# Kernel tuning notes

Hardware: AMD Instinct MI355X
Metric: run time of the kernel (lower is better)

The kernel has to match this reference:

```python
import jax, jax.numpy as jnp
import numpy as np

B, T, S, D, H, HD, DFF, NB = 2, 2048, 2048, 768, 12, 64, 3072, 32
HID = H * HD
EPS = 1e-6
NEG = -1e9


def rmsnorm(x, w):
    # T5 RMSNorm: no mean subtraction, no bias
    var = jnp.mean(jnp.square(x), axis=-1, keepdims=True)
    return x * jax.lax.rsqrt(var + EPS) * w


def sdpa(h, kv, m, wq, wk, wv, wo):
    # h: [B,Tq,D], kv: [B,Tk,D], m: additive mask broadcastable to [B,H,Tq,Tk]
    b, tq, _ = h.shape
    tk = kv.shape[1]
    q = (h @ wq).reshape(b, tq, H, HD)
    k = (kv @ wk).reshape(b, tk, H, HD)
    v = (kv @ wv).reshape(b, tk, H, HD)
    scores = jnp.einsum('bthd,bshd->bhts', q, k) + m  # scale=1.0 (T5)
    p = jax.nn.softmax(scores, axis=-1)
    y = jnp.einsum('bhts,bshd->bthd', p, v).reshape(b, tq, HID)
    return y @ wo


def setup_inputs() -> dict:
    key = jax.random.key(0)
    ks = jax.random.split(key, 16)
    x = jax.random.normal(ks[0], (B, T, D), dtype=jnp.float32)
    # causal additive mask for decoder self-attention
    causal = jnp.tril(jnp.ones((T, T), dtype=bool))
    mask = jnp.broadcast_to(jnp.where(causal, 0.0, NEG)[None, None], (B, 1, T, T)).astype(jnp.float32)
    relative_position = jax.random.randint(ks[1], (1, 1, T, T), 0, NB)
    encoder_hidden_states = jax.random.normal(ks[2], (B, S, D), dtype=jnp.float32)
    encoder_attention_mask = jnp.zeros((B, 1, T, S), dtype=jnp.float32)
    sc = 0.02
    p = {
        'sn_w': jnp.ones((D,), jnp.float32),
        'wq': sc * jax.random.normal(ks[3], (D, HID)),
        'wk': sc * jax.random.normal(ks[4], (D, HID)),
        'wv': sc * jax.random.normal(ks[5], (D, HID)),
        'wo': sc * jax.random.normal(ks[6], (HID, D)),
        'rel_emb': sc * jax.random.normal(ks[7], (NB, H)),
        'cn_w': jnp.ones((D,), jnp.float32),
        'cwq': sc * jax.random.normal(ks[8], (D, HID)),
        'cwk': sc * jax.random.normal(ks[9], (D, HID)),
        'cwv': sc * jax.random.normal(ks[10], (D, HID)),
        'cwo': sc * jax.random.normal(ks[11], (HID, D)),
        'pn_w': jnp.ones((D,), jnp.float32),
        'ffn_wi': sc * jax.random.normal(ks[12], (D, DFF)),
        'ffn_wo': sc * jax.random.normal(ks[13], (DFF, D)),
    }
    return dict(x=x, mask=mask, relative_position=relative_position,
                encoder_hidden_states=encoder_hidden_states,
                encoder_attention_mask=encoder_attention_mask, **p)


def reference(x, mask, relative_position, encoder_hidden_states, encoder_attention_mask,
              sn_w, wq, wk, wv, wo, rel_emb, cn_w, cwq, cwk, cwv, cwo, pn_w, ffn_wi, ffn_wo):
    # self-attention with relative-position bias added into additive mask
    h = rmsnorm(x, sn_w)
    # rel_emb[relative_position]: [1,1,T,T,H] -> permute(0,1,4,2,3) -> squeeze(0) -> [1,H,T,T]
    position_bias = jnp.transpose(rel_emb[relative_position], (0, 1, 4, 2, 3))[0]
    self_mask = mask + position_bias
    y = sdpa(h, h, self_mask, wq, wk, wv, wo)
    attn_out = y + x
    # cross-attention (no relative bias -> zeros position bias)
    enc_dec_position_bias = jnp.zeros_like(encoder_attention_mask)
    h2 = rmsnorm(attn_out, cn_w)
    y2 = sdpa(h2, encoder_hidden_states, encoder_attention_mask + enc_dec_position_bias,
              cwq, cwk, cwv, cwo)
    attn_out = y2 + attn_out
    # T5 FFN: relu(x @ wi) @ wo, pre-norm, residual
    hn = rmsnorm(attn_out, pn_w)
    ff = jax.nn.relu(hn @ ffn_wi) @ ffn_wo
    return (attn_out + ff, position_bias, enc_dec_position_bias)
```

## Files before the change

kernel.cpp:

```cpp
#include <hip/hip_runtime.h>
#include <hip/hip_bf16.h>
#include <stdint.h>

#define T5_B   2
#define T5_T   2048
#define T5_S   2048
#define T5_D   768
#define T5_H   12
#define T5_HD  64
#define T5_DFF 3072
#define T5_NB  32
#define NROW   4096

typedef __attribute__((ext_vector_type(8))) short bf16x8;
typedef __attribute__((ext_vector_type(4))) short short4v;
typedef __attribute__((ext_vector_type(4))) float f32x4;

__device__ __forceinline__ unsigned short f2bf(float x) {
  unsigned int u = __float_as_uint(x);
  unsigned int r = (u + 0x7FFFu + ((u >> 16) & 1u)) >> 16;
  return (unsigned short)r;
}

__device__ __forceinline__ void load_lds16(const void* g, void* l) {
  __builtin_amdgcn_global_load_lds(
      (__attribute__((address_space(1))) void*)(const_cast<void*>(g)),
      (__attribute__((address_space(3))) void*)(l), 16, 0, 0);
}

__device__ __forceinline__ unsigned cvt_pk_bf16(float lo_, float hi_) {
  unsigned d;
  asm("v_cvt_pk_bf16_f32 %0, %1, %2" : "=v"(d) : "v"(lo_), "v"(hi_));
  return d;
}

__device__ __forceinline__ f32x4 mfma16(short4v a, short4v b, f32x4 c) {
#if __has_builtin(__builtin_amdgcn_mfma_f32_16x16x16bf16_1k)
  return __builtin_amdgcn_mfma_f32_16x16x16bf16_1k(a, b, c, 0, 0, 0);
#else
  asm volatile("v_mfma_f32_16x16x16_bf16 %0, %1, %2, %0" : "+v"(c) : "v"(a), "v"(b));
  return c;
#endif
}

__device__ __forceinline__ int xcd_swz(int f, int nwg) {
  int q8 = nwg >> 3, r8 = nwg & 7, xcd = f & 7, base = f >> 3;
  return (xcd < r8 ? xcd * (q8 + 1) : r8 * (q8 + 1) + (xcd - r8) * q8) + base;
}

template <int TM, int TN, int EPI, int NBUF>
__device__ __forceinline__ void gemm_body(
    int f, int gx, int nwg,
    const unsigned short* __restrict__ A, const unsigned short* __restrict__ Bt,
    void* __restrict__ C, const float* __restrict__ res, int N, int K,
    unsigned short* LDS, unsigned short* vtp = nullptr, int vcol0 = 0) {
  constexpr int WR = (TM >= 128) ? 2 : 1;
  constexpr int WC = 4 / WR;
  constexpr int AM = TM / WR / 16;
  constexpr int AN = TN / WC / 16;
  constexpr int CHA = TM / 8, CHB = TN / 8, CPW = (CHA + CHB) / 4;
  constexpr int BUFSH = (TM + TN) * 64;
  constexpr int DEPTH = NBUF - 1;
  const int tid = threadIdx.x, lane = tid & 63, wv = tid >> 6;
  const int lo = lane & 15, hi = lane >> 4;
  const int wr = wv / WC, wc = wv % WC;
  const int wg = xcd_swz(f, nwg);
  const int m0 = (wg / gx) * TM, n0 = (wg % gx) * TN;

  f32x4 acc[AM][AN];
#pragma unroll
  for (int i = 0; i < AM; ++i)
#pragma unroll
    for (int j = 0; j < AN; ++j) acc[i][j] = f32x4{0.f, 0.f, 0.f, 0.f};

  const int srr  = lane >> 3;
  const int scol = ((lane & 7) ^ srr) * 8;

  auto stage = [&](int k0, int bsel) {
    unsigned short* Ab = LDS + bsel * BUFSH;
    unsigned short* Bb = Ab + TM * 64;
#pragma unroll
    for (int j = 0; j < CPW; ++j) {
      int c = wv * CPW + j;
      if (c < CHA)
        load_lds16(A + (size_t)(m0 + c * 8 + srr) * K + k0 + scol, Ab + c * 512);
      else {
        int c2 = c - CHA;
        load_lds16(Bt + (size_t)(n0 + c2 * 8 + srr) * K + k0 + scol, Bb + c2 * 512);
      }
    }
  };

  const int nIt = K >> 6;
#pragma unroll
  for (int p = 0; p < DEPTH; ++p)
    if (p < nIt) stage(p << 6, p % NBUF);

  for (int it = 0; it < nIt; ++it) {
    const int bsel = it % NBUF;
    if (it + DEPTH < nIt) {
      stage((it + DEPTH) << 6, (it + DEPTH) % NBUF);
      asm volatile("s_waitcnt vmcnt(%0)" :: "n"(DEPTH * CPW) : "memory");
    } else if (it + 1 < nIt) {
      asm volatile("s_waitcnt vmcnt(%0)" :: "n"(CPW) : "memory");
    } else {
      asm volatile("s_waitcnt vmcnt(0)" ::: "memory");
    }
    __builtin_amdgcn_s_barrier();
    __builtin_amdgcn_sched_barrier(0);
    const unsigned short* Ab = LDS + bsel * BUFSH;
    const unsigned short* Bb = Ab + TM * 64;
#pragma unroll
    for (int kk = 0; kk < 2; ++kk) {
      bf16x8 af[AM], bfr[AN];
#pragma unroll
      for (int i = 0; i < AM; ++i) {
        int row = wr * (AM * 16) + i * 16 + lo;
        unsigned by = (unsigned)(row * 128) + ((unsigned)(((kk * 4 + hi) ^ (row & 7))) << 4);
        af[i] = *(const bf16x8*)((const char*)Ab + by);
      }
#pragma unroll
      for (int j = 0; j < AN; ++j) {
        int row = wc * (AN * 16) + j * 16 + lo;
        unsigned by = (unsigned)(row * 128) + ((unsigned)(((kk * 4 + hi) ^ (row & 7))) << 4);
        bfr[j] = *(const bf16x8*)((const char*)Bb + by);
      }
      __builtin_amdgcn_s_setprio(1);
#pragma unroll
      for (int i = 0; i < AM; ++i)
#pragma unroll
        for (int j = 0; j < AN; ++j)
          acc[i][j] = __builtin_amdgcn_mfma_f32_16x16x32_bf16(af[i], bfr[j], acc[i][j], 0, 0, 0);
      __builtin_amdgcn_s_setprio(0);
    }
    __builtin_amdgcn_sched_barrier(0);
    __builtin_amdgcn_s_barrier();
  }

#pragma unroll
  for (int mi = 0; mi < AM; ++mi)
#pragma unroll
    for (int ni = 0; ni < AN; ++ni) {
      int row = m0 + wr * (AM * 16) + mi * 16 + hi * 4;
      int col = n0 + wc * (AN * 16) + ni * 16 + lo;
      if (EPI == 3 && col >= vcol0) {
        int cc = col - vcol0, hh = cc >> 6, dd = cc & 63;
        int bb = row >> 11, tt = row & 2047;
        unsigned long long pk = (unsigned long long)f2bf(acc[mi][ni][0])
                              | ((unsigned long long)f2bf(acc[mi][ni][1]) << 16)
                              | ((unsigned long long)f2bf(acc[mi][ni][2]) << 32)
                              | ((unsigned long long)f2bf(acc[mi][ni][3]) << 48);
        *(unsigned long long*)(vtp + ((size_t)((bb * 12 + hh) * 64 + dd)) * 2048 + tt) = pk;
      } else {
#pragma unroll
        for (int r = 0; r < 4; ++r) {
          float v = acc[mi][ni][r];
          size_t idx = (size_t)(row + r) * N + col;
          if (EPI == 0 || EPI == 3) {
            ((unsigned short*)C)[idx] = f2bf(v);
          } else if (EPI == 1) {
            ((float*)C)[idx] = v + res[idx];
          } else {
            ((unsigned short*)C)[idx] = f2bf(fmaxf(v, 0.0f));
          }
        }
      }
    }
}

template <int TM, int TN, int EPI, int NBUF>
__global__ __launch_bounds__(256)
void gemm_bt(const unsigned short* __restrict__ A, const unsigned short* __restrict__ Bt,
             void* __restrict__ C, const float* __restrict__ res, int N, int K) {
  __shared__ __align__(16) unsigned short LDS[NBUF * (TM + TN) * 64];
  int f = blockIdx.y * gridDim.x + blockIdx.x;
  gemm_body<TM, TN, EPI, NBUF>(f, gridDim.x, gridDim.x * gridDim.y, A, Bt, C, res, N, K, LDS);
}

struct PrepArgs {
  const float* wsrc[10];
  unsigned short* wdst[10];
  const float* enc; unsigned short* encb;
  const int* rp; unsigned char* rp8;
  const float* x; const float* snw; unsigned short* normb;
};

__global__ __launch_bounds__(256)
void prep_kernel(PrepArgs a) {
  __shared__ __align__(16) float tile[32][33];
  const int bid = blockIdx.x, tid = threadIdx.x;
  if (bid < 9216) {
    int widx, rem, Kd, Nd;
    if (bid < 4608)      { widx = bid / 576; rem = bid % 576;  Kd = 768;  Nd = 768;  }
    else if (bid < 6912) { widx = 8;         rem = bid - 4608; Kd = 768;  Nd = 3072; }
    else                 { widx = 9;         rem = bid - 6912; Kd = 3072; Nd = 768;  }
    const float* W = a.wsrc[widx];
    unsigned short* Wt = a.wdst[widx];
    int nb = Nd / 32;
    int n0 = (rem % nb) * 32, k0 = (rem / nb) * 32;
    int tx = tid & 31, ty = tid >> 5;
#pragma unroll
    for (int i = 0; i < 32; i += 8)
      tile[ty + i][tx] = W[(size_t)(k0 + ty + i) * Nd + n0 + tx];
    __syncthreads();
#pragma unroll
    for (int i = 0; i < 32; i += 8)
      Wt[(size_t)(n0 + ty + i) * Kd + k0 + tx] = f2bf(tile[tx][ty + i]);
  } else if (bid < 12288) {
    int i = (bid - 9216) * 256 + tid;
    float4 v = ((const float4*)a.enc)[i];
    unsigned long long pk = (unsigned long long)f2bf(v.x)
                          | ((unsigned long long)f2bf(v.y) << 16)
                          | ((unsigned long long)f2bf(v.z) << 32)
                          | ((unsigned long long)f2bf(v.w) << 48);
    *(unsigned long long*)(a.encb + (size_t)i * 4) = pk;
  } else if (bid < 13312) {
    int idx = (bid - 12288) * 256 + tid;
    const int4* src = (const int4*)(a.rp + (size_t)idx * 16);
    int4 v0 = src[0], v1 = src[1], v2 = src[2], v3 = src[3];
    uint4 o;
    o.x = (v0.x & 31) | ((v0.y & 31) << 8) | ((v0.z & 31) << 16) | ((v0.w & 31) << 24);
    o.y = (v1.x & 31) | ((v1.y & 31) << 8) | ((v1.z & 31) << 16) | ((v1.w & 31) << 24);
    o.z = (v2.x & 31) | ((v2.y & 31) << 8) | ((v2.z & 31) << 16) | ((v2.w & 31) << 24);
    o.w = (v3.x & 31) | ((v3.y & 31) << 8) | ((v3.z & 31) << 16) | ((v3.w & 31) << 24);
    ((uint4*)a.rp8)[idx] = o;
  } else {
    int row = bid - 13312;
    const float* r = a.x + (size_t)row * 768;
    float x0 = r[tid], x1 = r[tid + 256], x2 = r[tid + 512];
    float s = x0 * x0 + x1 * x1 + x2 * x2;
#pragma unroll
    for (int off = 32; off > 0; off >>= 1) s += __shfl_xor(s, off);
    float* wsm = &tile[0][0];
    int lane = tid & 63, wvv = tid >> 6;
    if (lane == 0) wsm[wvv] = s;
    __syncthreads();
    float tot = wsm[0] + wsm[1] + wsm[2] + wsm[3];
    float rinv = rsqrtf(tot * (1.0f / 768.0f) + 1e-6f);
    unsigned short* o = a.normb + (size_t)row * 768;
    o[tid]       = f2bf(x0 * rinv * a.snw[tid]);
    o[tid + 256] = f2bf(x1 * rinv * a.snw[tid + 256]);
    o[tid + 512] = f2bf(x2 * rinv * a.snw[tid + 512]);
  }
}

__global__ __launch_bounds__(256)
void rmsnorm_kernel(const float* __restrict__ in, const float* __restrict__ w,
                    unsigned short* __restrict__ out) {
  int row = blockIdx.x, tid = threadIdx.x;
  const float* r = in + (size_t)row * 768;
  float x0 = r[tid], x1 = r[tid + 256], x2 = r[tid + 512];
  float s = x0 * x0 + x1 * x1 + x2 * x2;
#pragma unroll
  for (int off = 32; off > 0; off >>= 1) s += __shfl_xor(s, off);
  __shared__ float ws_[4];
  int lane = tid & 63, wv = tid >> 6;
  if (lane == 0) ws_[wv] = s;
  __syncthreads();
  float tot = ws_[0] + ws_[1] + ws_[2] + ws_[3];
  float rinv = rsqrtf(tot * (1.0f / 768.0f) + 1e-6f);
  unsigned short* o = out + (size_t)row * 768;
  o[tid]       = f2bf(x0 * rinv * w[tid]);
  o[tid + 256] = f2bf(x1 * rinv * w[tid + 256]);
  o[tid + 512] = f2bf(x2 * rinv * w[tid + 512]);
}

struct Stage1Args {
  const unsigned short *normb, *wqkvT, *encb, *wckvT;
  unsigned short *qkv, *ckv, *vT1, *vT2;
  const int* rp; const float* rel;
  float *out1, *out2;
};

__global__ __launch_bounds__(256)
void stage1_kernel(Stage1Args a) {
  __shared__ __align__(16) unsigned short LDS[32768];
  const int bid = blockIdx.x, tid = threadIdx.x;
  if (bid < 576) {
    gemm_body<128, 128, 3, 2>(bid, 18, 576, a.normb, a.wqkvT, a.qkv, nullptr, 2304, 768,
                              LDS, a.vT1, 1536);
  } else if (bid < 960) {
    gemm_body<128, 128, 3, 2>(bid - 576, 12, 384, a.encb, a.wckvT, a.ckv, nullptr, 1536, 768,
                              LDS, a.vT2, 768);
  } else {
    const int p = bid - 960;
    float* rl = (float*)LDS;
    for (int i = tid; i < 384; i += 256) rl[i] = a.rel[i];
    __syncthreads();
    int t = p >> 1;
    int s = (p & 1) * 1024 + tid * 4;
    int4 nb = *(const int4*)(a.rp + (size_t)t * 2048 + s);
#pragma unroll
    for (int h = 0; h < 12; ++h) {
      float4 v = make_float4(rl[nb.x * 12 + h], rl[nb.y * 12 + h],
                             rl[nb.z * 12 + h], rl[nb.w * 12 + h]);
      *(float4*)(a.out1 + ((size_t)h * 2048 + t) * 2048 + s) = v;
    }
    size_t zbase = ((size_t)p * 256 + tid) * 8;
    float4 z = make_float4(0.f, 0.f, 0.f, 0.f);
    *(float4*)(a.out2 + zbase)     = z;
    *(float4*)(a.out2 + zbase + 4) = z;
  }
}

template <bool SELF>
__device__ __forceinline__ void attn_qcomp(
    const bf16x8& qf0, const bf16x8& qf1, f32x4* Oc, float& m_, float& l_,
    const unsigned* nb4, const float* rel_l, int qrow, bool edge, int s0,
    const unsigned short* Kb, const unsigned short* Vb, int lo, int hi) {
  f32x4 S[4];
  __builtin_amdgcn_s_setprio(1);
#pragma unroll
  for (int ct = 0; ct < 4; ++ct) {
    int krow = ct * 16 + lo;
    unsigned by0 = ((unsigned)(krow * 128 + hi * 16))      ^ ((unsigned)(krow & 7) << 4);
    unsigned by1 = ((unsigned)(krow * 128 + 64 + hi * 16)) ^ ((unsigned)(krow & 7) << 4);
    bf16x8 kf0 = *(const bf16x8*)((const char*)Kb + by0);
    bf16x8 kf1 = *(const bf16x8*)((const char*)Kb + by1);
    f32x4 sa = f32x4{0.f, 0.f, 0.f, 0.f};
    sa = __builtin_amdgcn_mfma_f32_16x16x32_bf16(kf0, qf0, sa, 0, 0, 0);
    sa = __builtin_amdgcn_mfma_f32_16x16x32_bf16(kf1, qf1, sa, 0, 0, 0);
    S[ct] = sa;
  }
  __builtin_amdgcn_s_setprio(0);

  if constexpr (SELF) {
#pragma unroll
    for (int ct = 0; ct < 4; ++ct) {
#pragma unroll
      for (int r = 0; r < 4; ++r) {
        int s = s0 + ct * 16 + hi * 4 + r;
        float sc = S[ct][r] + rel_l[(nb4[ct] >> (8 * r)) & 31u];
        if (edge && s > qrow) sc = -1e30f;
        S[ct][r] = sc;
      }
    }
  }

  float tm = S[0][0];
#pragma unroll
  for (int ct = 0; ct < 4; ++ct)
#pragma unroll
    for (int r = 0; r < 4; ++r) tm = fmaxf(tm, S[ct][r]);
  tm = fmaxf(tm, __shfl_xor(tm, 16));
  tm = fmaxf(tm, __shfl_xor(tm, 32));
  float mn = fmaxf(m_, tm);
  float alpha = __expf(m_ - mn);
  float rs = 0.f;
#pragma unroll
  for (int ct = 0; ct < 4; ++ct)
#pragma unroll
    for (int r = 0; r < 4; ++r) { float e = __expf(S[ct][r] - mn); S[ct][r] = e; rs += e; }
  rs += __shfl_xor(rs, 16);
  rs += __shfl_xor(rs, 32);
  l_ = l_ * alpha + rs;
  if (tm > m_) {
#pragma unroll
    for (int dt = 0; dt < 4; ++dt)
#pragma unroll
      for (int r = 0; r < 4; ++r) Oc[dt][r] *= alpha;
  }
  m_ = mn;

  short4v pf[4];
#pragma unroll
  for (int ct = 0; ct < 4; ++ct) {
    union { unsigned u[2]; short4v s; } cv;
    cv.u[0] = cvt_pk_bf16(S[ct][0], S[ct][1]);
    cv.u[1] = cvt_pk_bf16(S[ct][2], S[ct][3]);
    pf[ct] = cv.s;
  }

  __builtin_amdgcn_s_setprio(1);
#pragma unroll
  for (int dt = 0; dt < 4; ++dt) {
    int vrow = dt * 16 + lo;
#pragma unroll
    for (int ct = 0; ct < 4; ++ct) {
      unsigned vb = ((unsigned)(vrow * 128 + ct * 32 + hi * 8)) ^ ((unsigned)(vrow & 7) << 4);
      short4v vf = *(const short4v*)((const char*)Vb + vb);
      Oc[dt] = mfma16(vf, pf[ct], Oc[dt]);
    }
  }
  __builtin_amdgcn_s_setprio(0);
}

__device__ __forceinline__ void attn_store(f32x4* Oc, float l_, unsigned short* yr) {
  float inv = 1.0f / l_;
#pragma unroll
  for (int dt = 0; dt < 4; ++dt) {
    unsigned long long pk = (unsigned long long)f2bf(Oc[dt][0] * inv)
                          | ((unsigned long long)f2bf(Oc[dt][1] * inv) << 16)
                          | ((unsigned long long)f2bf(Oc[dt][2] * inv) << 32)
                          | ((unsigned long long)f2bf(Oc[dt][3] * inv) << 48);
    *(unsigned long long*)(yr + dt * 16) = pk;
  }
}

__global__ __launch_bounds__(256)
void attn_self_kernel(const unsigned short* __restrict__ qp,
                      const unsigned short* __restrict__ kp,
                      const unsigned short* __restrict__ vT,
                      const unsigned char* __restrict__ rp8,
                      const float* __restrict__ rel_emb,
                      unsigned short* __restrict__ yp) {
  __shared__ __align__(16) unsigned short Kls[2][4096];
  __shared__ __align__(16) unsigned short Vls[2][4096];
  __shared__ float rel_l[32];

  const int tid = threadIdx.x, lane = tid & 63, wv = tid >> 6;
  const int lo = lane & 15, hi = lane >> 4;
  const int wg = xcd_swz(blockIdx.x + 16 * (blockIdx.y + 12 * blockIdx.z), 384);
  const int xq = wg & 15, h = (wg >> 4) % 12, b = (wg >> 4) / 12;
  const int qta = xq, qtb = 31 - xq;
  const int ntiles = qtb + 1;

  if (tid < 32) rel_l[tid] = rel_emb[tid * 12 + h];

  const int qA = qta * 64 + wv * 16 + lo;
  const int qB = qtb * 64 + wv * 16 + lo;
  const unsigned short* qrA = qp + (size_t)(b * T5_T + qA) * 2304 + h * 64 + hi * 8;
  const unsigned short* qrB = qp + (size_t)(b * T5_T + qB) * 2304 + h * 64 + hi * 8;
  const bf16x8 qa0 = *(const bf16x8*)qrA;
  const bf16x8 qa1 = *(const bf16x8*)(qrA + 32);
  const bf16x8 qb0 = *(const bf16x8*)qrB;
  const bf16x8 qb1 = *(const bf16x8*)(qrB + 32);
  const unsigned char* rpqA = rp8 + (size_t)qA * 2048 + hi * 4;
  const unsigned char* rpqB = rp8 + (size_t)qB * 2048 + hi * 4;

  f32x4 OA[4], OB[4];
  float mA = -3.0e38f, lA = 0.f, mB = -3.0e38f, lB = 0.f;
#pragma unroll
  for (int i = 0; i < 4; ++i) { OA[i] = f32x4{0.f, 0.f, 0.f, 0.f}; OB[i] = f32x4{0.f, 0.f, 0.f, 0.f}; }

  const int krr = lane >> 3;
  const int kd0 = ((lane & 7) ^ krr) * 8;

  auto stage = [&](int kt, int bsel) {
    const int s0 = kt * 64;
#pragma unroll
    for (int j = 0; j < 2; ++j) {
      int c = wv * 2 + j;
      int rr = c * 8 + krr;
      load_lds16(kp + (size_t)(b * 2048 + s0 + rr) * 2304 + h * 64 + kd0, &Kls[bsel][c * 512]);
      load_lds16(vT + (size_t)((b * 12 + h) * 64 + rr) * 2048 + s0 + kd0,  &Vls[bsel][c * 512]);
    }
  };

  stage(0, 0);

  for (int kt = 0; kt < ntiles; ++kt) {
    const int bsel = kt & 1;
    const int s0 = kt * 64;
    asm volatile("s_waitcnt vmcnt(0)" ::: "memory");
    __syncthreads();
    unsigned nbA[4], nbB[4];
    if (kt <= qta) {
#pragma unroll
      for (int ct = 0; ct < 4; ++ct) nbA[ct] = *(const unsigned*)(rpqA + s0 + ct * 16);
    }
#pragma unroll
    for (int ct = 0; ct < 4; ++ct) nbB[ct] = *(const unsigned*)(rpqB + s0 + ct * 16);
    if (kt + 1 < ntiles) stage(kt + 1, bsel ^ 1);

    const unsigned short* Kb = &Kls[bsel][0];
    const unsigned short* Vb = &Vls[bsel][0];

    if (kt <= qta)
      attn_qcomp<true>(qa0, qa1, OA, mA, lA, nbA, rel_l, qA, kt == qta, s0, Kb, Vb, lo, hi);
    attn_qcomp<true>(qb0, qb1, OB, mB, lB, nbB, rel_l, qB, kt == qtb, s0, Kb, Vb, lo, hi);
  }

#if !__has_builtin(__builtin_amdgcn_mfma_f32_16x16x16bf16_1k)
  asm volatile("s_nop 7\n\ts_nop 7" ::: );
#endif

  attn_store(OA, lA, yp + (size_t)(b * T5_T + qA) * 768 + h * 64 + hi * 4);
  attn_store(OB, lB, yp + (size_t)(b * T5_T + qB) * 768 + h * 64 + hi * 4);
}

__global__ __launch_bounds__(256)
void attn_cross_kernel(const unsigned short* __restrict__ qp,
                       const unsigned short* __restrict__ kp,
                       const unsigned short* __restrict__ vT,
                       unsigned short* __restrict__ yp) {
  __shared__ __align__(16) unsigned short Kls[2][4096];
  __shared__ __align__(16) unsigned short Vls[2][4096];

  const int tid = threadIdx.x, lane = tid & 63, wv = tid >> 6;
  const int lo = lane & 15, hi = lane >> 4;
  const int wg = xcd_swz(blockIdx.x + 32 * (blockIdx.y + 12 * blockIdx.z), 768);
  const int xq = wg & 31, h = (wg >> 5) % 12, b = (wg >> 5) / 12;

  const int q = xq * 64 + wv * 16 + lo;
  const unsigned short* qr = qp + (size_t)(b * T5_T + q) * 768 + h * 64 + hi * 8;
  const bf16x8 qf0 = *(const bf16x8*)qr;
  const bf16x8 qf1 = *(const bf16x8*)(qr + 32);

  f32x4 Oc[4];
  float m_ = -3.0e38f, l_ = 0.f;
#pragma unroll
  for (int i = 0; i < 4; ++i) Oc[i] = f32x4{0.f, 0.f, 0.f, 0.f};

  const int krr = lane >> 3;
  const int kd0 = ((lane & 7) ^ krr) * 8;

  auto stage = [&](int kt, int bsel) {
    const int s0 = kt * 64;
#pragma unroll
    for (int j = 0; j < 2; ++j) {
      int c = wv * 2 + j;
      int rr = c * 8 + krr;
      load_lds16(kp + (size_t)(b * 2048 + s0 + rr) * 1536 + h * 64 + kd0, &Kls[bsel][c * 512]);
      load_lds16(vT + (size_t)((b * 12 + h) * 64 + rr) * 2048 + s0 + kd0, &Vls[bsel][c * 512]);
    }
  };

  stage(0, 0);

  for (int kt = 0; kt < 32; ++kt) {
    const int bsel = kt & 1;
    asm volatile("s_waitcnt vmcnt(0)" ::: "memory");
    __syncthreads();
    if (kt + 1 < 32) stage(kt + 1, bsel ^ 1);
    attn_qcomp<false>(qf0, qf1, Oc, m_, l_, nullptr, nullptr, 0, false, kt * 64,
                      &Kls[bsel][0], &Vls[bsel][0], lo, hi);
  }

#if !__has_builtin(__builtin_amdgcn_mfma_f32_16x16x16bf16_1k)
  asm volatile("s_nop 7\n\ts_nop 7" ::: );
#endif

  attn_store(Oc, l_, yp + (size_t)(b * T5_T + q) * 768 + h * 64 + hi * 4);
}

extern "C" void kernel_launch(void* const* d_in, const int* in_sizes, int n_in,
                              void* d_out, int out_size, void* d_ws, size_t ws_size,
                              hipStream_t stream) {
  (void)in_sizes; (void)n_in; (void)out_size; (void)ws_size;
  const float* x    = (const float*)d_in[0];
  const int*   rp   = (const int*)d_in[2];
  const float* enc  = (const float*)d_in[3];
  const float* sn_w = (const float*)d_in[5];
  const float* wq   = (const float*)d_in[6];
  const float* wk   = (const float*)d_in[7];
  const float* wvw  = (const float*)d_in[8];
  const float* wo   = (const float*)d_in[9];
  const float* rel  = (const float*)d_in[10];
  const float* cn_w = (const float*)d_in[11];
  const float* cwq  = (const float*)d_in[12];
  const float* cwk  = (const float*)d_in[13];
  const float* cwv  = (const float*)d_in[14];
  const float* cwo  = (const float*)d_in[15];
  const float* pn_w = (const float*)d_in[16];
  const float* wi   = (const float*)d_in[17];
  const float* wo2  = (const float*)d_in[18];

  float* out0 = (float*)d_out;
  float* out1 = out0 + (size_t)NROW * T5_D;
  float* out2 = out1 + (size_t)T5_H * T5_T * T5_T;

  char* ws = (char*)d_ws;
  size_t off = 0;
  auto alloc = [&](size_t bytes) { char* p = ws + off; off += (bytes + 255) & ~(size_t)255; return p; };
  unsigned short* wqkvT = (unsigned short*)alloc((size_t)2304 * 768 * 2);
  unsigned short* woT   = (unsigned short*)alloc((size_t)768 * 768 * 2);
  unsigned short* wckvT = (unsigned short*)alloc((size_t)1536 * 768 * 2);
  unsigned short* wcqT  = (unsigned short*)alloc((size_t)768 * 768 * 2);
  unsigned short* wcoT  = (unsigned short*)alloc((size_t)768 * 768 * 2);
  unsigned short* wiT   = (unsigned short*)alloc((size_t)3072 * 768 * 2);
  unsigned short* woT2  = (unsigned short*)alloc((size_t)768 * 3072 * 2);
  unsigned short* normb = (unsigned short*)alloc((size_t)NROW * 768 * 2);
  unsigned short* encb  = (unsigned short*)alloc((size_t)NROW * 768 * 2);
  unsigned short* ybuf  = (unsigned short*)alloc((size_t)NROW * 768 * 2);
  unsigned short* cq    = (unsigned short*)alloc((size_t)NROW * 768 * 2);
  float*          attn  = (float*)alloc((size_t)NROW * 768 * 4);
  unsigned char*  rp8p  = (unsigned char*)alloc((size_t)2048 * 2048);
  unsigned short* qkv   = (unsigned short*)alloc((size_t)NROW * 2304 * 2);
  unsigned short* ckv   = (unsigned short*)alloc((size_t)NROW * 1536 * 2);
  unsigned short* vT1   = (unsigned short*)alloc((size_t)24 * 64 * 2048 * 2);
  unsigned short* vT2   = (unsigned short*)alloc((size_t)24 * 64 * 2048 * 2);
  unsigned short* ffh   = (unsigned short*)alloc((size_t)NROW * 3072 * 2);

  dim3 blk(256);

  {
    PrepArgs pa;
    pa.wsrc[0] = wq;  pa.wdst[0] = wqkvT;
    pa.wsrc[1] = wk;  pa.wdst[1] = wqkvT + 768 * 768;
    pa.wsrc[2] = wvw; pa.wdst[2] = wqkvT + 2 * 768 * 768;
    pa.wsrc[3] = wo;  pa.wdst[3] = woT;
    pa.wsrc[4] = cwk; pa.wdst[4] = wckvT;
    pa.wsrc[5] = cwv; pa.wdst[5] = wckvT + 768 * 768;
    pa.wsrc[6] = cwq; pa.wdst[6] = wcqT;
    pa.wsrc[7] = cwo; pa.wdst[7] = wcoT;
    pa.wsrc[8] = wi;  pa.wdst[8] = wiT;
    pa.wsrc[9] = wo2; pa.wdst[9] = woT2;
    pa.enc = enc; pa.encb = encb; pa.rp = rp; pa.rp8 = rp8p;
    pa.x = x; pa.snw = sn_w; pa.normb = normb;
    prep_kernel<<<17408, blk, 0, stream>>>(pa);
  }

  {
    Stage1Args sa;
    sa.normb = normb; sa.wqkvT = wqkvT; sa.encb = encb; sa.wckvT = wckvT;
    sa.qkv = qkv; sa.ckv = ckv; sa.vT1 = vT1; sa.vT2 = vT2;
    sa.rp = rp; sa.rel = rel; sa.out1 = out1; sa.out2 = out2;
    stage1_kernel<<<5056, blk, 0, stream>>>(sa);
  }

  attn_self_kernel<<<dim3(16, 12, 2), blk, 0, stream>>>(qkv, qkv + 768, vT1, rp8p, rel, ybuf);
  gemm_bt<64, 64, 1, 3><<<dim3(12, 64), blk, 0, stream>>>(ybuf, woT, attn, x, 768, 768);

  rmsnorm_kernel<<<NROW, blk, 0, stream>>>(attn, cn_w, normb);
  gemm_bt<64, 64, 0, 3><<<dim3(12, 64), blk, 0, stream>>>(normb, wcqT, cq, nullptr, 768, 768);
  attn_cross_kernel<<<dim3(32, 12, 2), blk, 0, stream>>>(cq, ckv, vT2, ybuf);
  gemm_bt<64, 64, 1, 3><<<dim3(12, 64), blk, 0, stream>>>(ybuf, wcoT, attn, attn, 768, 768);

  rmsnorm_kernel<<<NROW, blk, 0, stream>>>(attn, pn_w, normb);
  gemm_bt<128, 128, 2, 2><<<dim3(24, 32), blk, 0, stream>>>(normb, wiT, ffh, nullptr, 3072, 768);
  gemm_bt<64, 64, 1, 3><<<dim3(12, 64), blk, 0, stream>>>(ffh, woT2, out0, attn, 768, 3072);
}
```

Baseline: 352.2 us.

## Use 32x32 MFMA for large GEMM tiles and fold log2e into Q for exp2 softmax

GEMMs with 128x128 tiles now use the 32x32x16 bf16 MFMA with a 2x2 accumulator layout per wave, instead of 16x16x32 fragments. This is meant to cut LDS fragment reads and instruction count per unit of work. Separately, Q projections (self and cross) and the relative-position bias table are pre-scaled by log2(e) in their epilogues, so the attention softmax can call raw v_exp_f32 instead of __expf. This removes a multiply per exponential, at the cost of bf16 rounding on the pre-scaled Q.

```diff
diff --git a/kernel.cpp b/kernel.cpp
--- a/kernel.cpp
+++ b/kernel.cpp
@@ -12,14 +12,23 @@
 #define T5_NB  32
 #define NROW   4096
 
+#define LOG2E 1.4426950408889634f
+
 typedef __attribute__((ext_vector_type(8))) short bf16x8;
 typedef __attribute__((ext_vector_type(4))) short short4v;
 typedef __attribute__((ext_vector_type(4))) float f32x4;
+typedef __attribute__((ext_vector_type(16))) float f32x16;
 
 __device__ __forceinline__ unsigned short f2bf(float x) {
   unsigned int u = __float_as_uint(x);
   unsigned int r = (u + 0x7FFFu + ((u >> 16) & 1u)) >> 16;
   return (unsigned short)r;
+}
+
+__device__ __forceinline__ float fexp2(float x) {
+  float d;
+  asm("v_exp_f32 %0, %1" : "=v"(d) : "v"(x));
+  return d;
 }
 
 __device__ __forceinline__ void load_lds16(const void* g, void* l) {
@@ -53,7 +62,8 @@
     int f, int gx, int nwg,
     const unsigned short* __restrict__ A, const unsigned short* __restrict__ Bt,
     void* __restrict__ C, const float* __restrict__ res, int N, int K,
-    unsigned short* LDS, unsigned short* vtp = nullptr, int vcol0 = 0) {
+    unsigned short* LDS, unsigned short* vtp = nullptr, int vcol0 = 0, int qe = 0) {
+  constexpr bool USE32 = (TM >= 128 && TN >= 128);
   constexpr int WR = (TM >= 128) ? 2 : 1;
   constexpr int WC = 4 / WR;
   constexpr int AM = TM / WR / 16;
@@ -63,15 +73,26 @@
   constexpr int DEPTH = NBUF - 1;
   const int tid = threadIdx.x, lane = tid & 63, wv = tid >> 6;
   const int lo = lane & 15, hi = lane >> 4;
+  const int l5 = lane >> 5, l31 = lane & 31;
   const int wr = wv / WC, wc = wv % WC;
   const int wg = xcd_swz(f, nwg);
   const int m0 = (wg / gx) * TM, n0 = (wg % gx) * TN;
 
-  f32x4 acc[AM][AN];
-#pragma unroll
-  for (int i = 0; i < AM; ++i)
-#pragma unroll
-    for (int j = 0; j < AN; ++j) acc[i][j] = f32x4{0.f, 0.f, 0.f, 0.f};
+  f32x4 acc[USE32 ? 1 : AM][USE32 ? 1 : AN];
+  f32x16 acc32[USE32 ? 2 : 1][USE32 ? 2 : 1];
+  if (USE32) {
+#pragma unroll
+    for (int i = 0; i < (USE32 ? 2 : 1); ++i)
+#pragma unroll
+      for (int j = 0; j < (USE32 ? 2 : 1); ++j)
+#pragma unroll
+        for (int r = 0; r < 16; ++r) acc32[i][j][r] = 0.f;
+  } else {
+#pragma unroll
+    for (int i = 0; i < (USE32 ? 1 : AM); ++i)
+#pragma unroll
+      for (int j = 0; j < (USE32 ? 1 : AN); ++j) acc[i][j] = f32x4{0.f, 0.f, 0.f, 0.f};
+  }
 
   const int srr  = lane >> 3;
   const int scol = ((lane & 7) ^ srr) * 8;
@@ -110,48 +131,104 @@
     __builtin_amdgcn_sched_barrier(0);
     const unsigned short* Ab = LDS + bsel * BUFSH;
     const unsigned short* Bb = Ab + TM * 64;
-#pragma unroll
-    for (int kk = 0; kk < 2; ++kk) {
-      bf16x8 af[AM], bfr[AN];
-#pragma unroll
-      for (int i = 0; i < AM; ++i) {
-        int row = wr * (AM * 16) + i * 16 + lo;
-        unsigned by = (unsigned)(row * 128) + ((unsigned)(((kk * 4 + hi) ^ (row & 7))) << 4);
-        af[i] = *(const bf16x8*)((const char*)Ab + by);
+    if (USE32) {
+#pragma unroll
+      for (int kk = 0; kk < 4; ++kk) {
+        bf16x8 af[2], bfr[2];
+#pragma unroll
+        for (int i = 0; i < 2; ++i) {
+          int row = wr * 64 + i * 32 + l31;
+          unsigned by = (unsigned)(row * 128) + ((unsigned)(((kk * 2 + l5) ^ (row & 7))) << 4);
+          af[i] = *(const bf16x8*)((const char*)Ab + by);
+        }
+#pragma unroll
+        for (int j = 0; j < 2; ++j) {
+          int row = wc * 64 + j * 32 + l31;
+          unsigned by = (unsigned)(row * 128) + ((unsigned)(((kk * 2 + l5) ^ (row & 7))) << 4);
+          bfr[j] = *(const bf16x8*)((const char*)Bb + by);
+        }
+        __builtin_amdgcn_s_setprio(1);
+#pragma unroll
+        for (int i = 0; i < 2; ++i)
+#pragma unroll
+          for (int j = 0; j < 2; ++j)
+            acc32[i][j] = __builtin_amdgcn_mfma_f32_32x32x16_bf16(af[i], bfr[j], acc32[i][j], 0, 0, 0);
+        __builtin_amdgcn_s_setprio(0);
       }
-#pragma unroll
-      for (int j = 0; j < AN; ++j) {
-        int row = wc * (AN * 16) + j * 16 + lo;
-        unsigned by = (unsigned)(row * 128) + ((unsigned)(((kk * 4 + hi) ^ (row & 7))) << 4);
-        bfr[j] = *(const bf16x8*)((const char*)Bb + by);
+    } else {
+#pragma unroll
+      for (int kk = 0; kk < 2; ++kk) {
+        bf16x8 af[AM], bfr[AN];
+#pragma unroll
+        for (int i = 0; i < AM; ++i) {
+          int row = wr * (AM * 16) + i * 16 + lo;
+          unsigned by = (unsigned)(row * 128) + ((unsigned)(((kk * 4 + hi) ^ (row & 7))) << 4);
+          af[i] = *(const bf16x8*)((const char*)Ab + by);
+        }
+#pragma unroll
+        for (int j = 0; j < AN; ++j) {
+          int row = wc * (AN * 16) + j * 16 + lo;
+          unsigned by = (unsigned)(row * 128) + ((unsigned)(((kk * 4 + hi) ^ (row & 7))) << 4);
+          bfr[j] = *(const bf16x8*)((const char*)Bb + by);
+        }
+        __builtin_amdgcn_s_setprio(1);
+#pragma unroll
+        for (int i = 0; i < AM; ++i)
+#pragma unroll
+          for (int j = 0; j < AN; ++j)
+            acc[i][j] = __builtin_amdgcn_mfma_f32_16x16x32_bf16(af[i], bfr[j], acc[i][j], 0, 0, 0);
+        __builtin_amdgcn_s_setprio(0);
       }
-      __builtin_amdgcn_s_setprio(1);
-#pragma unroll
-      for (int i = 0; i < AM; ++i)
-#pragma unroll
-        for (int j = 0; j < AN; ++j)
-          acc[i][j] = __builtin_amdgcn_mfma_f32_16x16x32_bf16(af[i], bfr[j], acc[i][j], 0, 0, 0);
-      __builtin_amdgcn_s_setprio(0);
     }
     __builtin_amdgcn_sched_barrier(0);
     __builtin_amdgcn_s_barrier();
   }
 
-#pragma unroll
-  for (int mi = 0; mi < AM; ++mi)
-#pragma unroll
-    for (int ni = 0; ni < AN; ++ni) {
-      int row = m0 + wr * (AM * 16) + mi * 16 + hi * 4;
-      int col = n0 + wc * (AN * 16) + ni * 16 + lo;
-      if (EPI == 3 && col >= vcol0) {
-        int cc = col - vcol0, hh = cc >> 6, dd = cc & 63;
-        int bb = row >> 11, tt = row & 2047;
-        unsigned long long pk = (unsigned long long)f2bf(acc[mi][ni][0])
-                              | ((unsigned long long)f2bf(acc[mi][ni][1]) << 16)
-                              | ((unsigned long long)f2bf(acc[mi][ni][2]) << 32)
-                              | ((unsigned long long)f2bf(acc[mi][ni][3]) << 48);
-        *(unsigned long long*)(vtp + ((size_t)((bb * 12 + hh) * 64 + dd)) * 2048 + tt) = pk;
-      } else {
+  if (USE32) {
+#pragma unroll
+    for (int i = 0; i < 2; ++i)
+#pragma unroll
+      for (int j = 0; j < 2; ++j) {
+        int colb = n0 + wc * 64 + j * 32 + l31;
+#pragma unroll
+        for (int g = 0; g < 4; ++g) {
+          int rowb = m0 + wr * 64 + i * 32 + g * 8 + 4 * l5;
+          if (EPI == 3 && colb >= vcol0) {
+            int cc = colb - vcol0, hh = cc >> 6, dd = cc & 63;
+            int bb = rowb >> 11, tt = rowb & 2047;
+            unsigned long long pk = (unsigned long long)f2bf(acc32[i][j][g * 4 + 0])
+                                  | ((unsigned long long)f2bf(acc32[i][j][g * 4 + 1]) << 16)
+                                  | ((unsigned long long)f2bf(acc32[i][j][g * 4 + 2]) << 32)
+                                  | ((unsigned long long)f2bf(acc32[i][j][g * 4 + 3]) << 48);
+            *(unsigned long long*)(vtp + ((size_t)((bb * 12 + hh) * 64 + dd)) * 2048 + tt) = pk;
+          } else {
+#pragma unroll
+            for (int rr = 0; rr < 4; ++rr) {
+              float v = acc32[i][j][g * 4 + rr];
+              size_t idx = (size_t)(rowb + rr) * N + colb;
+              if (EPI == 3) {
+                if (colb < qe) v *= LOG2E;
+                ((unsigned short*)C)[idx] = f2bf(v);
+              } else if (EPI == 0) {
+                ((unsigned short*)C)[idx] = f2bf(v);
+              } else if (EPI == 1) {
+                ((float*)C)[idx] = v + res[idx];
+              } else if (EPI == 2) {
+                ((unsigned short*)C)[idx] = f2bf(fmaxf(v, 0.0f));
+              } else {
+                ((unsigned short*)C)[idx] = f2bf(v * LOG2E);
+              }
+            }
+          }
+        }
+      }
+  } else {
+#pragma unroll
+    for (int mi = 0; mi < (USE32 ? 1 : AM); ++mi)
+#pragma unroll
+      for (int ni = 0; ni < (USE32 ? 1 : AN); ++ni) {
+        int row = m0 + wr * (AM * 16) + mi * 16 + hi * 4;
+        int col = n0 + wc * (AN * 16) + ni * 16 + lo;
 #pragma unroll
         for (int r = 0; r < 4; ++r) {
           float v = acc[mi][ni][r];
@@ -160,12 +237,14 @@
             ((unsigned short*)C)[idx] = f2bf(v);
           } else if (EPI == 1) {
             ((float*)C)[idx] = v + res[idx];
+          } else if (EPI == 2) {
+            ((unsigned short*)C)[idx] = f2bf(fmaxf(v, 0.0f));
           } else {
-            ((unsigned short*)C)[idx] = f2bf(fmaxf(v, 0.0f));
+            ((unsigned short*)C)[idx] = f2bf(v * LOG2E);
           }
         }
       }
-    }
+  }
 }
 
 template <int TM, int TN, int EPI, int NBUF>
@@ -278,10 +357,10 @@
   const int bid = blockIdx.x, tid = threadIdx.x;
   if (bid < 576) {
     gemm_body<128, 128, 3, 2>(bid, 18, 576, a.normb, a.wqkvT, a.qkv, nullptr, 2304, 768,
-                              LDS, a.vT1, 1536);
+                              LDS, a.vT1, 1536, 768);
   } else if (bid < 960) {
     gemm_body<128, 128, 3, 2>(bid - 576, 12, 384, a.encb, a.wckvT, a.ckv, nullptr, 1536, 768,
-                              LDS, a.vT2, 768);
+                              LDS, a.vT2, 768, 0);
   } else {
     const int p = bid - 960;
     float* rl = (float*)LDS;
@@ -345,12 +424,12 @@
   tm = fmaxf(tm, __shfl_xor(tm, 16));
   tm = fmaxf(tm, __shfl_xor(tm, 32));
   float mn = fmaxf(m_, tm);
-  float alpha = __expf(m_ - mn);
+  float alpha = fexp2(m_ - mn);
   float rs = 0.f;
 #pragma unroll
   for (int ct = 0; ct < 4; ++ct)
 #pragma unroll
-    for (int r = 0; r < 4; ++r) { float e = __expf(S[ct][r] - mn); S[ct][r] = e; rs += e; }
+    for (int r = 0; r < 4; ++r) { float e = fexp2(S[ct][r] - mn); S[ct][r] = e; rs += e; }
   rs += __shfl_xor(rs, 16);
   rs += __shfl_xor(rs, 32);
   l_ = l_ * alpha + rs;
@@ -415,7 +494,7 @@
   const int qta = xq, qtb = 31 - xq;
   const int ntiles = qtb + 1;
 
-  if (tid < 32) rel_l[tid] = rel_emb[tid * 12 + h];
+  if (tid < 32) rel_l[tid] = rel_emb[tid * 12 + h] * LOG2E;
 
   const int qA = qta * 64 + wv * 16 + lo;
   const int qB = qtb * 64 + wv * 16 + lo;
@@ -613,7 +692,7 @@
   gemm_bt<64, 64, 1, 3><<<dim3(12, 64), blk, 0, stream>>>(ybuf, woT, attn, x, 768, 768);
 
   rmsnorm_kernel<<<NROW, blk, 0, stream>>>(attn, cn_w, normb);
-  gemm_bt<64, 64, 0, 3><<<dim3(12, 64), blk, 0, stream>>>(normb, wcqT, cq, nullptr, 768, 768);
+  gemm_bt<64, 64, 4, 3><<<dim3(12, 64), blk, 0, stream>>>(normb, wcqT, cq, nullptr, 768, 768);
   attn_cross_kernel<<<dim3(32, 12, 2), blk, 0, stream>>>(cq, ckv, vT2, ybuf);
   gemm_bt<64, 64, 1, 3><<<dim3(12, 64), blk, 0, stream>>>(ybuf, wcoT, attn, attn, 768, 768);
 
```

After: 350.0 us. Within noise of the previous version (-0.6%).
